# Kernel optimization log

Measured on AMD Instinct MI355X. Metric: run time of the kernel, lower is better.

The kernel has to match this reference:

```python
import jax, jax.numpy as jnp
import numpy as np

C = 192   # channels (class attr)
N = 196   # tokens per stream; 2N = 392, R feat dim = 784
B = 256

def _pw(x, w, b):
    # 1x1 Conv1d == pointwise channel mix: x [B,Ci,L] -> [B,Co,L]
    return jnp.einsum('oi,bil->bol', w, x) + b[None, :, None]

def _bn(x, g, beta, m, v):
    # eval-mode BatchNorm1d
    inv = g / jnp.sqrt(v + 1e-5)
    return (x - m[None, :, None]) * inv[None, :, None] + beta[None, :, None]

def setup_inputs():
    key = jax.random.key(0)
    ks = jax.random.split(key, 24)
    s = 1.0 / np.sqrt(C)
    d = {}
    d['x'] = jax.random.normal(ks[0], (B, N, C), dtype=jnp.float32)
    d['y'] = jax.random.normal(ks[1], (B, N, C), dtype=jnp.float32)
    # linear_conv_1: Conv1d(C,C,1) + BN + ReLU
    d['w1'] = jax.random.normal(ks[2], (C, C), dtype=jnp.float32) * s
    d['b1'] = jax.random.normal(ks[3], (C,), dtype=jnp.float32) * 0.01
    d['g1'] = jnp.ones((C,), jnp.float32)
    d['be1'] = jnp.zeros((C,), jnp.float32)
    d['m1'] = jax.random.normal(ks[4], (C,), dtype=jnp.float32) * 0.1
    d['v1'] = jax.random.uniform(ks[5], (C,), dtype=jnp.float32) + 0.5
    # linear_conv_2
    d['w2'] = jax.random.normal(ks[6], (C, C), dtype=jnp.float32) * s
    d['b2'] = jax.random.normal(ks[7], (C,), dtype=jnp.float32) * 0.01
    d['g2'] = jnp.ones((C,), jnp.float32)
    d['be2'] = jnp.zeros((C,), jnp.float32)
    d['m2'] = jax.random.normal(ks[8], (C,), dtype=jnp.float32) * 0.1
    d['v2'] = jax.random.uniform(ks[9], (C,), dtype=jnp.float32) + 0.5
    # linear_conv_3: Conv1d(C,C,1)
    d['w3'] = jax.random.normal(ks[10], (C, C), dtype=jnp.float32) * s
    d['b3'] = jax.random.normal(ks[11], (C,), dtype=jnp.float32) * 0.01
    # linear_conv_4: Conv1d(784,784,1)
    d['w4'] = jax.random.normal(ks[12], (784, 784), dtype=jnp.float32) / np.sqrt(784)
    d['b4'] = jax.random.normal(ks[13], (784,), dtype=jnp.float32) * 0.01
    # linear_conv_5: Conv1d(C+784,1,1)
    d['w5'] = jax.random.normal(ks[14], (1, C + 784), dtype=jnp.float32) / np.sqrt(C + 784)
    d['b5'] = jax.random.normal(ks[15], (1,), dtype=jnp.float32) * 0.01
    return d

def reference(x, y, w1, b1, g1, be1, m1, v1, w2, b2, g2, be2, m2, v2, w3, b3, w4, b4, w5, b5):
    xp = jnp.swapaxes(x, 1, 2)  # [B,C,N]
    yp = jnp.swapaxes(y, 1, 2)
    phi_x = jax.nn.relu(_bn(_pw(xp, w1, b1), g1, be1, m1, v1))
    phi_y = jax.nn.relu(_bn(_pw(yp, w2, b2), g2, be2, m2, v2))
    cat_phi = jnp.concatenate([phi_x, phi_y], axis=2)            # [B,C,2N]
    A = jnp.einsum('bcn,bcm->bnm', cat_phi, cat_phi)             # [B,2N,2N]
    # R[b,i,:] = cat(A[b,i,:], A[b,:,i]) for i in 0..2N-1, then permute(0,2,1)
    R = jnp.concatenate([A, jnp.swapaxes(A, 1, 2)], axis=2)      # [B,2N,4N]
    R = jnp.swapaxes(R, 1, 2)                                    # [B,4N,2N] = [B,784,392]
    v = _pw(cat_phi, w3, b3)                                     # [B,C,392]
    v_ = _pw(R, w4, b4)                                          # [B,784,392]
    cat_v = jnp.concatenate([v, v_], axis=1)                     # [B,976,392]
    W = _pw(cat_v, w5, b5)                                       # [B,1,392]
    out = xp * W[:, :, :N] + yp * W[:, :, N:]                    # [B,C,N]
    return out
```

## Files before the change

### kernel.cpp

```cpp
#include <hip/hip_runtime.h>
#include <hip/hip_bf16.h>

typedef __attribute__((ext_vector_type(8))) short bf16x8;
typedef __attribute__((ext_vector_type(4))) float f32x4;

#define CDIM 192
#define NTOK 196
#define LTOT 392
#define NBE 64

__device__ __forceinline__ ushort f2bf(float f) {
  uint u = __float_as_uint(f);
  u = (u + 0x7FFFu + ((u >> 16) & 1u)) >> 16;
  return (ushort)u;
}
__device__ __forceinline__ float bf2f(ushort h) {
  return __uint_as_float(((uint)h) << 16);
}
__device__ __forceinline__ uint pk2(float lo, float hi) {
  __hip_bfloat162 t = __float22bfloat162_rn(float2{lo, hi});
  uint r;
  __builtin_memcpy(&r, &t, 4);
  return r;
}
__device__ __forceinline__ float wave_reduce(float a) {
#pragma unroll
  for (int off = 32; off > 0; off >>= 1) a += __shfl_xor(a, off);
  return a;
}
__device__ __forceinline__ void barL() {
  asm volatile("s_waitcnt lgkmcnt(0)" ::: "memory");
  __builtin_amdgcn_s_barrier();
  __builtin_amdgcn_sched_barrier(0);
}

__global__ __launch_bounds__(256) void prep_kernel(
    const float* __restrict__ w1, const float* __restrict__ b1, const float* __restrict__ g1,
    const float* __restrict__ be1, const float* __restrict__ m1, const float* __restrict__ v1,
    const float* __restrict__ w2, const float* __restrict__ b2, const float* __restrict__ g2,
    const float* __restrict__ be2, const float* __restrict__ m2, const float* __restrict__ v2,
    const float* __restrict__ w3, const float* __restrict__ b3,
    const float* __restrict__ w4, const float* __restrict__ b4,
    const float* __restrict__ w5, const float* __restrict__ b5,
    ushort* __restrict__ w1b, ushort* __restrict__ w2b,
    float* __restrict__ u3, float* __restrict__ u4, float* __restrict__ cvecs,
    float* __restrict__ Kc) {
  const int bid = blockIdx.x;
  const int wid = threadIdx.x >> 6, lane = threadIdx.x & 63;
  if (bid < NBE) {
    for (int i = bid * 256 + threadIdx.x; i < 74112; i += NBE * 256) {
      if (i < 36864) {
        int o = i / CDIM;
        float inv = g1[o] * rsqrtf(v1[o] + 1e-5f);
        w1b[i] = f2bf(w1[i] * inv);
      } else if (i < 73728) {
        int j = i - 36864; int o = j / CDIM;
        float inv = g2[o] * rsqrtf(v2[o] + 1e-5f);
        w2b[j] = f2bf(w2[j] * inv);
      } else {
        int k = i - 73728; int h = k / CDIM, o = k % CDIM;
        const float* bb = h ? b2 : b1; const float* gg = h ? g2 : g1;
        const float* bee = h ? be2 : be1;
        const float* mm = h ? m2 : m1; const float* vv = h ? v2 : v1;
        float inv = gg[o] * rsqrtf(vv[o] + 1e-5f);
        cvecs[k] = (bb[o] - mm[o]) * inv + bee[o];
      }
    }
  } else if (bid < NBE + 48) {
    int j = (bid - NBE) * 4 + wid;
    float a = 0.f;
    for (int c = lane; c < CDIM; c += 64) a += w5[c] * w3[c * CDIM + j];
    a = wave_reduce(a);
    if (lane == 0) u3[j] = a;
  } else if (bid < NBE + 48 + 98) {
    int j = (bid - NBE - 48) * 4 + wid;
    float a = 0.f;
    for (int o = lane; o < 784; o += 64)
      a += w5[CDIM + o] * (w4[o * 784 + j] + w4[o * 784 + j + LTOT]);
    a = wave_reduce(a);
    if (lane == 0) u4[j] = a;
  } else {
    if (wid == 0) {
      float a = 0.f;
      for (int i = lane; i < CDIM + 784; i += 64)
        a += (i < CDIM) ? w5[i] * b3[i] : w5[i] * b4[i - CDIM];
      a = wave_reduce(a);
      if (lane == 0) Kc[0] = a + b5[0];
    }
  }
}

#define PHIL_BYTES (404 * 384)
#define OFF_U4S PHIL_BYTES
#define OFF_CSL (OFF_U4S + 1632)
#define OFF_SARR (OFF_CSL + 1536)
#define OFF_WL (OFF_SARR + 768)
#define SMEM_BYTES (OFF_WL + 1568)

extern __shared__ char smem[];

__global__ __launch_bounds__(768, 1) void fused_kernel(
    const float* __restrict__ x, const float* __restrict__ y,
    const ushort* __restrict__ w1b, const ushort* __restrict__ w2b,
    const float* __restrict__ cvecs, const float* __restrict__ u4,
    const float* __restrict__ u3, const float* __restrict__ Kc,
    float* __restrict__ out) {
  const int b = blockIdx.x;
  ushort* phiL = (ushort*)smem;
  float* u4s = (float*)(smem + OFF_U4S);
  float* csL = (float*)(smem + OFF_CSL);
  float* sArr = (float*)(smem + OFF_SARR);
  float* Wl = (float*)(smem + OFF_WL);
  const int tid = threadIdx.x;
  for (int i = tid; i < 408; i += 768) u4s[i] = (i < LTOT) ? u4[i] : 0.f;
  for (int i = tid; i < 384; i += 768) csL[i] = cvecs[i];

  const int w = tid >> 6, lane = tid & 63;
  const int lrow = lane & 15, kgrp = lane >> 4;
  const int c = w * 16 + lrow;

  bf16x8 bfr0[6], bfr1[6];
#pragma unroll
  for (int kk = 0; kk < 6; kk++) {
    bfr0[kk] = *(const bf16x8*)(w1b + (size_t)c * CDIM + kk * 32 + kgrp * 8);
    bfr1[kk] = *(const bf16x8*)(w2b + (size_t)c * CDIM + kk * 32 + kgrp * 8);
  }
  barL();
  const float csr0 = csL[c], csr1 = csL[CDIM + c];

  const float4* xb4 = (const float4*)(x + (size_t)b * NTOK * CDIM);
  const float4* yb4 = (const float4*)(y + (size_t)b * NTOK * CDIM);
  float sp = 0.f;

  auto loadpf = [&](int R, float4* pf) {
    if (R < 8) {
      const float4* s4 = (R < 4) ? xb4 : yb4;
      const int base = (R & 3) * 3072;
#pragma unroll
      for (int p = 0; p < 4; p++) {
        const int fi = base + p * 768 + tid;
        pf[p] = (fi < 9408) ? s4[fi] : float4{0.f, 0.f, 0.f, 0.f};
      }
    }
  };
  float4 pfA[4], pfB[4];
  loadpf(0, pfA);
  loadpf(1, pfB);

  for (int R = 0; R < 8; R++) {
    const int h = R >> 2, r = R & 3;
#pragma unroll
    for (int p = 0; p < 4; p++) {
      const int fi = r * 3072 + p * 768 + tid;
      if (fi < 9408) {
        const int row = fi / 48, c4 = fi - row * 48;
        const int l = h * NTOK + row;
        uint2 wv;
        wv.x = pk2(pfA[p].x, pfA[p].y);
        wv.y = pk2(pfA[p].z, pfA[p].w);
        uint addr = (uint)(l * 384 + c4 * 8) ^ (uint)((l & 7) << 4);
        *(uint2*)((char*)phiL + addr) = wv;
      }
    }
#pragma unroll
    for (int p = 0; p < 4; p++) pfA[p] = pfB[p];
    loadpf(R + 2, pfB);
    barL();

    f32x4 acc[4];
#pragma unroll
    for (int tt = 0; tt < 4; tt++) acc[tt] = f32x4{0.f, 0.f, 0.f, 0.f};
#pragma unroll
    for (int tt = 0; tt < 4; tt++) {
      const int rb = r * 64 + tt * 16;
      if (rb < NTOK) {
        bf16x8 af[6];
        const int l0 = h * NTOK + rb + lrow;
#pragma unroll
        for (int kk = 0; kk < 6; kk++) {
          uint ad = (uint)(l0 * 384 + (kk * 32 + kgrp * 8) * 2) ^ (uint)((l0 & 7) << 4);
          af[kk] = *(const bf16x8*)((const char*)phiL + ad);
        }
        if (h == 0) {
#pragma unroll
          for (int kk = 0; kk < 6; kk++)
            acc[tt] = __builtin_amdgcn_mfma_f32_16x16x32_bf16(af[kk], bfr0[kk], acc[tt], 0, 0, 0);
        } else {
#pragma unroll
          for (int kk = 0; kk < 6; kk++)
            acc[tt] = __builtin_amdgcn_mfma_f32_16x16x32_bf16(af[kk], bfr1[kk], acc[tt], 0, 0, 0);
        }
      }
    }
    barL();

    const float csr = h ? csr1 : csr0;
#pragma unroll
    for (int tt = 0; tt < 4; tt++) {
      const int rb = r * 64 + tt * 16;
      if (rb < NTOK) {
        const float v0 = fmaxf(acc[tt][0] + csr, 0.f);
        const float v1 = fmaxf(acc[tt][1] + csr, 0.f);
        const float v2 = fmaxf(acc[tt][2] + csr, 0.f);
        const float v3 = fmaxf(acc[tt][3] + csr, 0.f);
        const uint p01 = pk2(v0, v1), p23 = pk2(v2, v3);
        const int row0 = rb + 4 * kgrp;
#pragma unroll
        for (int j = 0; j < 4; j++) {
          const int row = row0 + j;
          if (row < NTOK) {
            const int l = h * NTOK + row;
            uint addr = (uint)(l * 384 + c * 2) ^ (uint)((l & 7) << 4);
            const uint piece = (j == 0) ? (p01 & 0xFFFFu) : (j == 1) ? (p01 >> 16)
                             : (j == 2) ? (p23 & 0xFFFFu) : (p23 >> 16);
            *(ushort*)((char*)phiL + addr) = (ushort)piece;
            const float vj = (j == 0) ? v0 : (j == 1) ? v1 : (j == 2) ? v2 : v3;
            sp += u4s[l] * vj;
          }
        }
      }
    }
  }

  sp += __shfl_xor(sp, 16);
  sp += __shfl_xor(sp, 32);
  if (kgrp == 0) sArr[c] = sp;
  barL();
  for (int i = tid; i < CDIM; i += 768) sArr[i] = u3[i] + sArr[i];
  barL();

  const float Kv = Kc[0];
  const int grp = tid >> 2, g4 = tid & 3;
  for (int l = grp; l < LTOT; l += 192) {
    float acc = 0.f;
#pragma unroll
    for (int q = 0; q < 12; q++) {
      const int cc = g4 * 48 + q * 4;
      uint addr = (uint)(l * 384 + cc * 2) ^ (uint)((l & 7) << 4);
      ushort4 v = *(const ushort4*)((const char*)phiL + addr);
      acc += sArr[cc] * bf2f(v.x) + sArr[cc + 1] * bf2f(v.y) +
             sArr[cc + 2] * bf2f(v.z) + sArr[cc + 3] * bf2f(v.w);
    }
    acc += __shfl_xor(acc, 1);
    acc += __shfl_xor(acc, 2);
    if (g4 == 0) Wl[l] = acc + Kv;
  }

  float* tileF = (float*)smem;
  const float* xb = x + (size_t)b * NTOK * CDIM;
  const float* yb = y + (size_t)b * NTOK * CDIM;
  float4 px[2], py[2];
  auto loadT = [&](int nt) {
    if (nt < 7) {
#pragma unroll
      for (int p = 0; p < 2; p++) {
        const int i = p * 768 + tid;
        if (i < 1344) {
          const size_t xi = (size_t)(nt * 28 + i / 48) * CDIM + (i % 48) * 4;
          px[p] = *(const float4*)&xb[xi];
          py[p] = *(const float4*)&yb[xi];
        }
      }
    }
  };
  loadT(0);
  for (int nt = 0; nt < 7; nt++) {
    const int n0 = nt * 28;
    barL();
#pragma unroll
    for (int p = 0; p < 2; p++) {
      const int i = p * 768 + tid;
      if (i < 1344) {
        const int nl = i / 48, c4 = (i % 48) * 4;
        const float wx = Wl[n0 + nl], wy = Wl[NTOK + n0 + nl];
        tileF[nl * 193 + c4 + 0] = px[p].x * wx + py[p].x * wy;
        tileF[nl * 193 + c4 + 1] = px[p].y * wx + py[p].y * wy;
        tileF[nl * 193 + c4 + 2] = px[p].z * wx + py[p].z * wy;
        tileF[nl * 193 + c4 + 3] = px[p].w * wx + py[p].w * wy;
      }
    }
    loadT(nt + 1);
    barL();
#pragma unroll
    for (int p = 0; p < 2; p++) {
      const int i = p * 768 + tid;
      if (i < 1344) {
        const int cc = i / 7, nq = i % 7;
        float4 o;
        o.x = tileF[(nq * 4 + 0) * 193 + cc];
        o.y = tileF[(nq * 4 + 1) * 193 + cc];
        o.z = tileF[(nq * 4 + 2) * 193 + cc];
        o.w = tileF[(nq * 4 + 3) * 193 + cc];
        *(float4*)&out[((size_t)b * CDIM + cc) * NTOK + n0 + nq * 4] = o;
      }
    }
  }
}

extern "C" void kernel_launch(void* const* d_in, const int* in_sizes, int n_in,
                              void* d_out, int out_size, void* d_ws, size_t ws_size,
                              hipStream_t stream) {
  const float* x   = (const float*)d_in[0];
  const float* y   = (const float*)d_in[1];
  const float* w1  = (const float*)d_in[2];
  const float* b1  = (const float*)d_in[3];
  const float* g1  = (const float*)d_in[4];
  const float* be1 = (const float*)d_in[5];
  const float* m1  = (const float*)d_in[6];
  const float* v1  = (const float*)d_in[7];
  const float* w2  = (const float*)d_in[8];
  const float* b2  = (const float*)d_in[9];
  const float* g2  = (const float*)d_in[10];
  const float* be2 = (const float*)d_in[11];
  const float* m2  = (const float*)d_in[12];
  const float* v2  = (const float*)d_in[13];
  const float* w3  = (const float*)d_in[14];
  const float* b3  = (const float*)d_in[15];
  const float* w4  = (const float*)d_in[16];
  const float* b4  = (const float*)d_in[17];
  const float* w5  = (const float*)d_in[18];
  const float* b5  = (const float*)d_in[19];
  float* out = (float*)d_out;

  char* ws = (char*)d_ws;
  ushort* w1b  = (ushort*)ws;
  ushort* w2b  = (ushort*)(ws + 73728);
  float* fbase = (float*)(ws + 147456);
  float* u3    = fbase;
  float* u4    = fbase + 192;
  float* cvecs = fbase + 584;
  float* Kc    = fbase + 968;

  prep_kernel<<<211, 256, 0, stream>>>(w1, b1, g1, be1, m1, v1,
                                       w2, b2, g2, be2, m2, v2,
                                       w3, b3, w4, b4, w5, b5,
                                       w1b, w2b, u3, u4, cvecs, Kc);
  fused_kernel<<<256, 768, SMEM_BYTES, stream>>>(x, y, w1b, w2b, cvecs, u4,
                                                 u3, Kc, out);
}
```

Baseline: 61.37 us.

## Restructure phi stage into four large chunks with deeper prefetch and vectorized W pass

```diff
diff --git a/kernel.cpp b/kernel.cpp
--- a/kernel.cpp
+++ b/kernel.cpp
@@ -119,108 +119,98 @@
   const int lrow = lane & 15, kgrp = lane >> 4;
   const int c = w * 16 + lrow;
 
-  bf16x8 bfr0[6], bfr1[6];
-#pragma unroll
-  for (int kk = 0; kk < 6; kk++) {
-    bfr0[kk] = *(const bf16x8*)(w1b + (size_t)c * CDIM + kk * 32 + kgrp * 8);
-    bfr1[kk] = *(const bf16x8*)(w2b + (size_t)c * CDIM + kk * 32 + kgrp * 8);
-  }
-  barL();
-  const float csr0 = csL[c], csr1 = csL[CDIM + c];
+  bf16x8 bfr[6];
+#pragma unroll
+  for (int kk = 0; kk < 6; kk++)
+    bfr[kk] = *(const bf16x8*)(w1b + (size_t)c * CDIM + kk * 32 + kgrp * 8);
 
   const float4* xb4 = (const float4*)(x + (size_t)b * NTOK * CDIM);
   const float4* yb4 = (const float4*)(y + (size_t)b * NTOK * CDIM);
+  float4 pfA[7], pfB[6];
   float sp = 0.f;
 
-  auto loadpf = [&](int R, float4* pf) {
-    if (R < 8) {
-      const float4* s4 = (R < 4) ? xb4 : yb4;
-      const int base = (R & 3) * 3072;
-#pragma unroll
-      for (int p = 0; p < 4; p++) {
-        const int fi = base + p * 768 + tid;
-        pf[p] = (fi < 9408) ? s4[fi] : float4{0.f, 0.f, 0.f, 0.f};
-      }
-    }
-  };
-  float4 pfA[4], pfB[4];
-  loadpf(0, pfA);
-  loadpf(1, pfB);
-
-  for (int R = 0; R < 8; R++) {
-    const int h = R >> 2, r = R & 3;
-#pragma unroll
-    for (int p = 0; p < 4; p++) {
-      const int fi = r * 3072 + p * 768 + tid;
-      if (fi < 9408) {
-        const int row = fi / 48, c4 = fi - row * 48;
-        const int l = h * NTOK + row;
-        uint2 wv;
-        wv.x = pk2(pfA[p].x, pfA[p].y);
-        wv.y = pk2(pfA[p].z, pfA[p].w);
-        uint addr = (uint)(l * 384 + c4 * 8) ^ (uint)((l & 7) << 4);
-        *(uint2*)((char*)phiL + addr) = wv;
-      }
-    }
-#pragma unroll
-    for (int p = 0; p < 4; p++) pfA[p] = pfB[p];
-    loadpf(R + 2, pfB);
-    barL();
-
-    f32x4 acc[4];
-#pragma unroll
-    for (int tt = 0; tt < 4; tt++) acc[tt] = f32x4{0.f, 0.f, 0.f, 0.f};
-#pragma unroll
-    for (int tt = 0; tt < 4; tt++) {
-      const int rb = r * 64 + tt * 16;
-      if (rb < NTOK) {
-        bf16x8 af[6];
-        const int l0 = h * NTOK + rb + lrow;
-#pragma unroll
-        for (int kk = 0; kk < 6; kk++) {
-          uint ad = (uint)(l0 * 384 + (kk * 32 + kgrp * 8) * 2) ^ (uint)((l0 & 7) << 4);
-          af[kk] = *(const bf16x8*)((const char*)phiL + ad);
-        }
-        if (h == 0) {
-#pragma unroll
-          for (int kk = 0; kk < 6; kk++)
-            acc[tt] = __builtin_amdgcn_mfma_f32_16x16x32_bf16(af[kk], bfr0[kk], acc[tt], 0, 0, 0);
-        } else {
-#pragma unroll
-          for (int kk = 0; kk < 6; kk++)
-            acc[tt] = __builtin_amdgcn_mfma_f32_16x16x32_bf16(af[kk], bfr1[kk], acc[tt], 0, 0, 0);
-        }
-      }
-    }
-    barL();
-
-    const float csr = h ? csr1 : csr0;
-#pragma unroll
-    for (int tt = 0; tt < 4; tt++) {
-      const int rb = r * 64 + tt * 16;
-      if (rb < NTOK) {
-        const float v0 = fmaxf(acc[tt][0] + csr, 0.f);
-        const float v1 = fmaxf(acc[tt][1] + csr, 0.f);
-        const float v2 = fmaxf(acc[tt][2] + csr, 0.f);
-        const float v3 = fmaxf(acc[tt][3] + csr, 0.f);
-        const uint p01 = pk2(v0, v1), p23 = pk2(v2, v3);
-        const int row0 = rb + 4 * kgrp;
-#pragma unroll
-        for (int j = 0; j < 4; j++) {
-          const int row = row0 + j;
-          if (row < NTOK) {
-            const int l = h * NTOK + row;
-            uint addr = (uint)(l * 384 + c * 2) ^ (uint)((l & 7) << 4);
-            const uint piece = (j == 0) ? (p01 & 0xFFFFu) : (j == 1) ? (p01 >> 16)
-                             : (j == 2) ? (p23 & 0xFFFFu) : (p23 >> 16);
-            *(ushort*)((char*)phiL + addr) = (ushort)piece;
-            const float vj = (j == 0) ? v0 : (j == 1) ? v1 : (j == 2) ? v2 : v3;
-            sp += u4s[l] * vj;
-          }
-        }
-      }
-    }
-  }
+#define LOADC(PF, CNT, NF4, SRC4, ROW0) do {                                   \
+  _Pragma("unroll")                                                            \
+  for (int p = 0; p < (CNT); p++) {                                            \
+    const int fi = p * 768 + tid;                                              \
+    (PF)[p] = (fi < (NF4)) ? (SRC4)[(ROW0) * 48 + fi]                          \
+                           : float4{0.f, 0.f, 0.f, 0.f};                       \
+  } } while (0)
+
+#define STAGE(PF, CNT, NF4, H, ROW0) do {                                      \
+  _Pragma("unroll")                                                            \
+  for (int p = 0; p < (CNT); p++) {                                            \
+    const int fi = p * 768 + tid;                                              \
+    if (fi < (NF4)) {                                                          \
+      const int l = (H) * NTOK + (ROW0) + fi / 48;                             \
+      const int c4 = fi % 48;                                                  \
+      uint2 wv;                                                                \
+      wv.x = pk2((PF)[p].x, (PF)[p].y);                                        \
+      wv.y = pk2((PF)[p].z, (PF)[p].w);                                        \
+      uint addr = (uint)(l * 384 + c4 * 8) ^ (uint)((l & 7) << 4);             \
+      *(uint2*)((char*)phiL + addr) = wv;                                      \
+    } } } while (0)
+
+#define MFMA_EPI(H, ROW0, NT, CSR) do {                                        \
+  f32x4 acc[7];                                                                \
+  _Pragma("unroll")                                                            \
+  for (int tt = 0; tt < 7; tt++) acc[tt] = f32x4{0.f, 0.f, 0.f, 0.f};          \
+  _Pragma("unroll")                                                            \
+  for (int tt = 0; tt < 7; tt++) if (tt < (NT)) {                              \
+    const int l0 = (H) * NTOK + (ROW0) + tt * 16 + lrow;                       \
+    bf16x8 af[6];                                                              \
+    _Pragma("unroll")                                                          \
+    for (int kk = 0; kk < 6; kk++) {                                           \
+      uint ad = (uint)(l0 * 384 + kk * 64 + kgrp * 16) ^ (uint)((l0 & 7) << 4);\
+      af[kk] = *(const bf16x8*)((const char*)phiL + ad);                       \
+    }                                                                          \
+    _Pragma("unroll")                                                          \
+    for (int kk = 0; kk < 6; kk++)                                             \
+      acc[tt] = __builtin_amdgcn_mfma_f32_16x16x32_bf16(af[kk], bfr[kk],       \
+                                                        acc[tt], 0, 0, 0);    \
+  }                                                                            \
+  barL();                \
+  _Pragma("unroll")                                                            \
+  for (int tt = 0; tt < 7; tt++) if (tt < (NT)) {                              \
+    const float v0 = fmaxf(acc[tt][0] + (CSR), 0.f);                           \
+    const float v1 = fmaxf(acc[tt][1] + (CSR), 0.f);                           \
+    const float v2 = fmaxf(acc[tt][2] + (CSR), 0.f);                           \
+    const float v3 = fmaxf(acc[tt][3] + (CSR), 0.f);                           \
+    const uint p01 = pk2(v0, v1), p23 = pk2(v2, v3);                           \
+    const int rw0 = (ROW0) + tt * 16 + 4 * kgrp;                               \
+    _Pragma("unroll")                                                          \
+    for (int j = 0; j < 4; j++) {                                              \
+      const int row = rw0 + j;                                                 \
+      if (row < NTOK) {                                                        \
+        const int l = (H) * NTOK + row;                                        \
+        uint addr = (uint)(l * 384 + c * 2) ^ (uint)((l & 7) << 4);            \
+        const uint piece = (j == 0) ? (p01 & 0xFFFFu) : (j == 1) ? (p01 >> 16) \
+                         : (j == 2) ? (p23 & 0xFFFFu) : (p23 >> 16);           \
+        *(ushort*)((char*)phiL + addr) = (ushort)piece;                        \
+        const float vj = (j == 0) ? v0 : (j == 1) ? v1 : (j == 2) ? v2 : v3;   \
+        sp += u4s[l] * vj;                                                     \
+      } } } } while (0)
+
+  LOADC(pfA, 7, 5376, xb4, 0);
+  LOADC(pfB, 6, 4032, xb4, 112);
+  STAGE(pfA, 7, 5376, 0, 0);
+  LOADC(pfA, 7, 5376, yb4, 0);
+  barL();
+  const float csr0 = csL[c], csr1 = csL[CDIM + c];
+  MFMA_EPI(0, 0, 7, csr0);
+  STAGE(pfB, 6, 4032, 0, 112);
+  LOADC(pfB, 6, 4032, yb4, 112);
+  barL();
+  MFMA_EPI(0, 112, 6, csr0);
+#pragma unroll
+  for (int kk = 0; kk < 6; kk++)
+    bfr[kk] = *(const bf16x8*)(w2b + (size_t)c * CDIM + kk * 32 + kgrp * 8);
+  STAGE(pfA, 7, 5376, 1, 0);
+  barL();
+  MFMA_EPI(1, 0, 7, csr1);
+  STAGE(pfB, 6, 4032, 1, 112);
+  barL();
+  MFMA_EPI(1, 112, 6, csr1);
 
   sp += __shfl_xor(sp, 16);
   sp += __shfl_xor(sp, 32);
@@ -230,56 +220,67 @@
   barL();
 
   const float Kv = Kc[0];
-  const int grp = tid >> 2, g4 = tid & 3;
-  for (int l = grp; l < LTOT; l += 192) {
+#pragma unroll
+  for (int p = 0; p < 3; p++) {
+    const int row = p * 192 + w * 16 + lrow;
     float acc = 0.f;
-#pragma unroll
-    for (int q = 0; q < 12; q++) {
-      const int cc = g4 * 48 + q * 4;
-      uint addr = (uint)(l * 384 + cc * 2) ^ (uint)((l & 7) << 4);
-      ushort4 v = *(const ushort4*)((const char*)phiL + addr);
-      acc += sArr[cc] * bf2f(v.x) + sArr[cc + 1] * bf2f(v.y) +
-             sArr[cc + 2] * bf2f(v.z) + sArr[cc + 3] * bf2f(v.w);
+    if (row < LTOT) {
+#pragma unroll
+      for (int kk = 0; kk < 6; kk++) {
+        const int c0 = kk * 32 + kgrp * 8;
+        uint addr = (uint)(row * 384 + c0 * 2) ^ (uint)((row & 7) << 4);
+        const uint4 pv = *(const uint4*)((const char*)phiL + addr);
+        const float4 cfa = *(const float4*)&sArr[c0];
+        const float4 cfb = *(const float4*)&sArr[c0 + 4];
+        acc += cfa.x * bf2f((ushort)pv.x) + cfa.y * bf2f((ushort)(pv.x >> 16))
+             + cfa.z * bf2f((ushort)pv.y) + cfa.w * bf2f((ushort)(pv.y >> 16))
+             + cfb.x * bf2f((ushort)pv.z) + cfb.y * bf2f((ushort)(pv.z >> 16))
+             + cfb.z * bf2f((ushort)pv.w) + cfb.w * bf2f((ushort)(pv.w >> 16));
+      }
     }
-    acc += __shfl_xor(acc, 1);
-    acc += __shfl_xor(acc, 2);
-    if (g4 == 0) Wl[l] = acc + Kv;
+    acc += __shfl_xor(acc, 16);
+    acc += __shfl_xor(acc, 32);
+    if (kgrp == 0 && row < LTOT) Wl[row] = acc + Kv;
   }
 
   float* tileF = (float*)smem;
   const float* xb = x + (size_t)b * NTOK * CDIM;
   const float* yb = y + (size_t)b * NTOK * CDIM;
-  float4 px[2], py[2];
-  auto loadT = [&](int nt) {
-    if (nt < 7) {
-#pragma unroll
-      for (int p = 0; p < 2; p++) {
-        const int i = p * 768 + tid;
-        if (i < 1344) {
-          const size_t xi = (size_t)(nt * 28 + i / 48) * CDIM + (i % 48) * 4;
-          px[p] = *(const float4*)&xb[xi];
-          py[p] = *(const float4*)&yb[xi];
-        }
-      }
-    }
-  };
-  loadT(0);
+  float4 pxA[2], pyA[2], pxB[2], pyB[2];
+
+#define LOADT(NT, PX, PY) do {                                                 \
+  if ((NT) < 7) {                                                              \
+    _Pragma("unroll")                                                          \
+    for (int p = 0; p < 2; p++) {                                              \
+      const int i = p * 768 + tid;                                             \
+      if (i < 1344) {                                                          \
+        const size_t xi = (size_t)((NT) * 28 + i / 48) * CDIM + (i % 48) * 4;  \
+        (PX)[p] = *(const float4*)&xb[xi];                                     \
+        (PY)[p] = *(const float4*)&yb[xi];                                     \
+      } } } } while (0)
+
+#define COMBINE(N0, PX, PY) do {                                               \
+  _Pragma("unroll")                                                            \
+  for (int p = 0; p < 2; p++) {                                                \
+    const int i = p * 768 + tid;                                               \
+    if (i < 1344) {                                                            \
+      const int nl = i / 48, c4 = (i % 48) * 4;                                \
+      const float wx = Wl[(N0) + nl], wy = Wl[NTOK + (N0) + nl];               \
+      float4 o;                                                                \
+      o.x = (PX)[p].x * wx + (PY)[p].x * wy;                                   \
+      o.y = (PX)[p].y * wx + (PY)[p].y * wy;                                   \
+      o.z = (PX)[p].z * wx + (PY)[p].z * wy;                                   \
+      o.w = (PX)[p].w * wx + (PY)[p].w * wy;                                   \
+      *(float4*)&tileF[nl * 196 + c4] = o;                                     \
+    } } } while (0)
+
+  LOADT(0, pxA, pyA);
+  LOADT(1, pxB, pyB);
   for (int nt = 0; nt < 7; nt++) {
     const int n0 = nt * 28;
     barL();
-#pragma unroll
-    for (int p = 0; p < 2; p++) {
-      const int i = p * 768 + tid;
-      if (i < 1344) {
-        const int nl = i / 48, c4 = (i % 48) * 4;
-        const float wx = Wl[n0 + nl], wy = Wl[NTOK + n0 + nl];
-        tileF[nl * 193 + c4 + 0] = px[p].x * wx + py[p].x * wy;
-        tileF[nl * 193 + c4 + 1] = px[p].y * wx + py[p].y * wy;
-        tileF[nl * 193 + c4 + 2] = px[p].z * wx + py[p].z * wy;
-        tileF[nl * 193 + c4 + 3] = px[p].w * wx + py[p].w * wy;
-      }
-    }
-    loadT(nt + 1);
+    if (nt & 1) { COMBINE(n0, pxB, pyB); LOADT(nt + 2, pxB, pyB); }
+    else        { COMBINE(n0, pxA, pyA); LOADT(nt + 2, pxA, pyA); }
     barL();
 #pragma unroll
     for (int p = 0; p < 2; p++) {
@@ -287,10 +288,10 @@
       if (i < 1344) {
         const int cc = i / 7, nq = i % 7;
         float4 o;
-        o.x = tileF[(nq * 4 + 0) * 193 + cc];
-        o.y = tileF[(nq * 4 + 1) * 193 + cc];
-        o.z = tileF[(nq * 4 + 2) * 193 + cc];
-        o.w = tileF[(nq * 4 + 3) * 193 + cc];
+        o.x = tileF[(nq * 4 + 0) * 196 + cc];
+        o.y = tileF[(nq * 4 + 1) * 196 + cc];
+        o.z = tileF[(nq * 4 + 2) * 196 + cc];
+        o.w = tileF[(nq * 4 + 3) * 196 + cc];
         *(float4*)&out[((size_t)b * CDIM + cc) * NTOK + n0 + nq * 4] = o;
       }
     }
```

Result: no change. 61.11 us, median of 2 (-0.4%).

## Restructure fused kernel with 32x32 MFMA tiles, half-stream chunks, per-wave output transpose

Applied to the files above, without the earlier changes.

```diff
diff --git a/kernel.cpp b/kernel.cpp
--- a/kernel.cpp
+++ b/kernel.cpp
@@ -2,7 +2,7 @@
 #include <hip/hip_bf16.h>
 
 typedef __attribute__((ext_vector_type(8))) short bf16x8;
-typedef __attribute__((ext_vector_type(4))) float f32x4;
+typedef __attribute__((ext_vector_type(16))) float f32x16;
 
 #define CDIM 192
 #define NTOK 196
@@ -90,12 +90,12 @@
   }
 }
 
-#define PHIL_BYTES (404 * 384)
-#define OFF_U4S PHIL_BYTES
+#define OFF_WL 0
+#define OFF_PHIL 1568
+#define OFF_U4S (OFF_PHIL + 150528)
 #define OFF_CSL (OFF_U4S + 1632)
-#define OFF_SARR (OFF_CSL + 1536)
-#define OFF_WL (OFF_SARR + 768)
-#define SMEM_BYTES (OFF_WL + 1568)
+#define OFF_SA (OFF_CSL + 1536)
+#define SMEM_BYTES (OFF_SA + 1536)
 
 extern __shared__ char smem[];
 
@@ -106,192 +106,196 @@
     const float* __restrict__ u3, const float* __restrict__ Kc,
     float* __restrict__ out) {
   const int b = blockIdx.x;
-  ushort* phiL = (ushort*)smem;
+  float* Wl = (float*)(smem + OFF_WL);
+  char* phiB = smem + OFF_PHIL;
   float* u4s = (float*)(smem + OFF_U4S);
   float* csL = (float*)(smem + OFF_CSL);
-  float* sArr = (float*)(smem + OFF_SARR);
-  float* Wl = (float*)(smem + OFF_WL);
+  float* sA = (float*)(smem + OFF_SA);
   const int tid = threadIdx.x;
   for (int i = tid; i < 408; i += 768) u4s[i] = (i < LTOT) ? u4[i] : 0.f;
   for (int i = tid; i < 384; i += 768) csL[i] = cvecs[i];
 
   const int w = tid >> 6, lane = tid & 63;
-  const int lrow = lane & 15, kgrp = lane >> 4;
-  const int c = w * 16 + lrow;
-
-  bf16x8 bfr0[6], bfr1[6];
-#pragma unroll
-  for (int kk = 0; kk < 6; kk++) {
-    bfr0[kk] = *(const bf16x8*)(w1b + (size_t)c * CDIM + kk * 32 + kgrp * 8);
-    bfr1[kk] = *(const bf16x8*)(w2b + (size_t)c * CDIM + kk * 32 + kgrp * 8);
-  }
-  barL();
-  const float csr0 = csL[c], csr1 = csL[CDIM + c];
+  const int cw = w % 6, lg = w / 6;
+  const int cbase = cw * 32;
+  const int cl32 = lane & 31, hi = lane >> 5;
+  const int c = cbase + cl32;
+
+  bf16x8 bfr[12];
+#pragma unroll
+  for (int kk = 0; kk < 12; kk++)
+    bfr[kk] = *(const bf16x8*)(w1b + (size_t)c * CDIM + kk * 16 + hi * 8);
 
   const float4* xb4 = (const float4*)(x + (size_t)b * NTOK * CDIM);
   const float4* yb4 = (const float4*)(y + (size_t)b * NTOK * CDIM);
+  float4 pfA[6], pfB[7];
   float sp = 0.f;
 
-  auto loadpf = [&](int R, float4* pf) {
-    if (R < 8) {
-      const float4* s4 = (R < 4) ? xb4 : yb4;
-      const int base = (R & 3) * 3072;
-#pragma unroll
-      for (int p = 0; p < 4; p++) {
-        const int fi = base + p * 768 + tid;
-        pf[p] = (fi < 9408) ? s4[fi] : float4{0.f, 0.f, 0.f, 0.f};
-      }
-    }
-  };
-  float4 pfA[4], pfB[4];
-  loadpf(0, pfA);
-  loadpf(1, pfB);
-
-  for (int R = 0; R < 8; R++) {
-    const int h = R >> 2, r = R & 3;
-#pragma unroll
-    for (int p = 0; p < 4; p++) {
-      const int fi = r * 3072 + p * 768 + tid;
-      if (fi < 9408) {
-        const int row = fi / 48, c4 = fi - row * 48;
+  auto loadA = [&](const float4* s4) {
+#pragma unroll
+    for (int p = 0; p < 6; p++) pfA[p] = s4[p * 768 + tid];
+  };
+  auto loadB = [&](const float4* s4) {
+#pragma unroll
+    for (int p = 0; p < 7; p++) {
+      const int fi = p * 768 + tid;
+      pfB[p] = (fi < 4800) ? s4[4608 + fi] : float4{0.f, 0.f, 0.f, 0.f};
+    }
+  };
+  auto stageA = [&](int h) {
+#pragma unroll
+    for (int p = 0; p < 6; p++) {
+      const int fi = p * 768 + tid;
+      const int l = h * NTOK + fi / 48, c4 = fi % 48;
+      uint2 wv;
+      wv.x = pk2(pfA[p].x, pfA[p].y);
+      wv.y = pk2(pfA[p].z, pfA[p].w);
+      uint addr = (uint)(l * 384 + c4 * 8) ^ (uint)((l & 7) << 4);
+      *(uint2*)(phiB + addr) = wv;
+    }
+  };
+  auto stageB = [&](int h) {
+#pragma unroll
+    for (int p = 0; p < 7; p++) {
+      const int fi = p * 768 + tid;
+      if (fi < 4800) {
+        const int l = h * NTOK + 96 + fi / 48, c4 = fi % 48;
+        uint2 wv;
+        wv.x = pk2(pfB[p].x, pfB[p].y);
+        wv.y = pk2(pfB[p].z, pfB[p].w);
+        uint addr = (uint)(l * 384 + c4 * 8) ^ (uint)((l & 7) << 4);
+        *(uint2*)(phiB + addr) = wv;
+      }
+    }
+  };
+
+  auto tileMFMA = [&](int h, int l0) -> f32x16 {
+    f32x16 acc;
+#pragma unroll
+    for (int e = 0; e < 16; e++) acc[e] = 0.f;
+    const int l = h * NTOK + l0 + cl32;
+    const uint swz = (uint)((l & 7) << 4);
+#pragma unroll
+    for (int kk = 0; kk < 12; kk++) {
+      uint ad = (uint)(l * 384 + kk * 32 + hi * 16) ^ swz;
+      bf16x8 af = *(const bf16x8*)(phiB + ad);
+      acc = __builtin_amdgcn_mfma_f32_32x32x16_bf16(af, bfr[kk], acc, 0, 0, 0);
+    }
+    return acc;
+  };
+  auto tileEPI = [&](int h, int l0, const f32x16& acc, float csr, bool ovl) {
+#pragma unroll
+    for (int e = 0; e < 16; e++) {
+      const int rl = (e & 3) + 8 * (e >> 2) + 4 * hi;
+      const int row = l0 + rl;
+      if (!ovl || row >= 192) {
+        const float v = fmaxf(acc[e] + csr, 0.f);
         const int l = h * NTOK + row;
-        uint2 wv;
-        wv.x = pk2(pfA[p].x, pfA[p].y);
-        wv.y = pk2(pfA[p].z, pfA[p].w);
-        uint addr = (uint)(l * 384 + c4 * 8) ^ (uint)((l & 7) << 4);
-        *(uint2*)((char*)phiL + addr) = wv;
-      }
-    }
-#pragma unroll
-    for (int p = 0; p < 4; p++) pfA[p] = pfB[p];
-    loadpf(R + 2, pfB);
+        uint addr = (uint)(l * 384 + c * 2) ^ (uint)((l & 7) << 4);
+        *(ushort*)(phiB + addr) = f2bf(v);
+        sp += u4s[l] * v;
+      }
+    }
+  };
+  auto chunkCompute = [&](int h, int cb, float csr) {
+    const int l0s[2][4] = {{0, 32, 64, -1}, {96, 128, 160, 164}};
+    const int nt = cb ? 4 : 3;
+    f32x16 a0, a1;
+    const int t0 = lg, t1 = lg + 2;
+    if (t0 < nt) a0 = tileMFMA(h, l0s[cb][t0]);
+    if (t1 < nt) a1 = tileMFMA(h, l0s[cb][t1]);
     barL();
-
-    f32x4 acc[4];
-#pragma unroll
-    for (int tt = 0; tt < 4; tt++) acc[tt] = f32x4{0.f, 0.f, 0.f, 0.f};
-#pragma unroll
-    for (int tt = 0; tt < 4; tt++) {
-      const int rb = r * 64 + tt * 16;
-      if (rb < NTOK) {
-        bf16x8 af[6];
-        const int l0 = h * NTOK + rb + lrow;
+    if (t0 < nt) tileEPI(h, l0s[cb][t0], a0, csr, cb && l0s[cb][t0] == 164);
+    if (t1 < nt) tileEPI(h, l0s[cb][t1], a1, csr, cb && l0s[cb][t1] == 164);
+  };
+
+  loadA(xb4);
+  loadB(xb4);
+  stageA(0);
+  loadA(yb4);
+  barL();
+  const float csr0 = csL[c], csr1 = csL[CDIM + c];
+  chunkCompute(0, 0, csr0);
+  stageB(0);
+  loadB(yb4);
+  barL();
+  chunkCompute(0, 1, csr0);
+#pragma unroll
+  for (int kk = 0; kk < 12; kk++)
+    bfr[kk] = *(const bf16x8*)(w2b + (size_t)c * CDIM + kk * 16 + hi * 8);
+  stageA(1);
+  barL();
+  chunkCompute(1, 0, csr1);
+  stageB(1);
+  barL();
+  chunkCompute(1, 1, csr1);
+
+  sp += __shfl_xor(sp, 32);
+  if (hi == 0) sA[lg * CDIM + c] = sp;
+  barL();
+  for (int i = tid; i < CDIM; i += 768) sA[i] = u3[i] + sA[i] + sA[CDIM + i];
+  barL();
+
+  {
+    const float Kv = Kc[0];
+    const int lrow = lane & 15, kgrp = lane >> 4;
+#pragma unroll
+    for (int p = 0; p < 3; p++) {
+      const int row = p * 192 + w * 16 + lrow;
+      float acc = 0.f;
+      if (row < LTOT) {
 #pragma unroll
         for (int kk = 0; kk < 6; kk++) {
-          uint ad = (uint)(l0 * 384 + (kk * 32 + kgrp * 8) * 2) ^ (uint)((l0 & 7) << 4);
-          af[kk] = *(const bf16x8*)((const char*)phiL + ad);
+          const int c0 = kk * 32 + kgrp * 8;
+          uint addr = (uint)(row * 384 + c0 * 2) ^ (uint)((row & 7) << 4);
+          const uint4 pv = *(const uint4*)(phiB + addr);
+          const float4 cfa = *(const float4*)&sA[c0];
+          const float4 cfb = *(const float4*)&sA[c0 + 4];
+          acc += cfa.x * bf2f((ushort)pv.x) + cfa.y * bf2f((ushort)(pv.x >> 16))
+               + cfa.z * bf2f((ushort)pv.y) + cfa.w * bf2f((ushort)(pv.y >> 16))
+               + cfb.x * bf2f((ushort)pv.z) + cfb.y * bf2f((ushort)(pv.z >> 16))
+               + cfb.z * bf2f((ushort)pv.w) + cfb.w * bf2f((ushort)(pv.w >> 16));
         }
-        if (h == 0) {
-#pragma unroll
-          for (int kk = 0; kk < 6; kk++)
-            acc[tt] = __builtin_amdgcn_mfma_f32_16x16x32_bf16(af[kk], bfr0[kk], acc[tt], 0, 0, 0);
-        } else {
-#pragma unroll
-          for (int kk = 0; kk < 6; kk++)
-            acc[tt] = __builtin_amdgcn_mfma_f32_16x16x32_bf16(af[kk], bfr1[kk], acc[tt], 0, 0, 0);
+      }
+      acc += __shfl_xor(acc, 16);
+      acc += __shfl_xor(acc, 32);
+      if (kgrp == 0 && row < LTOT) Wl[row] = acc + Kv;
+    }
+  }
+  barL();
+
+  {
+    float* tf = (float*)(phiB + w * 4352);
+    const int cb16 = w * 16;
+    const float* xb = x + (size_t)b * NTOK * CDIM;
+    const float* yb = y + (size_t)b * NTOK * CDIM;
+    const int nrow = lane >> 2, cq = lane & 3;
+    const int scl = lane >> 2, sq = lane & 3;
+    for (int s0 = 0; s0 < 4; s0++) {
+      const int n0 = s0 * 64;
+#pragma unroll
+      for (int i2 = 0; i2 < 4; i2++) {
+        const int n = n0 + i2 * 16 + nrow;
+        if (n < NTOK) {
+          const size_t xi = (size_t)n * CDIM + cb16 + cq * 4;
+          const float4 xv = *(const float4*)&xb[xi];
+          const float4 yv = *(const float4*)&yb[xi];
+          const float wx = Wl[n], wy = Wl[NTOK + n];
+          const int dn = n - n0;
+          tf[(cq * 4 + 0) * 68 + dn] = xv.x * wx + yv.x * wy;
+          tf[(cq * 4 + 1) * 68 + dn] = xv.y * wx + yv.y * wy;
+          tf[(cq * 4 + 2) * 68 + dn] = xv.z * wx + yv.z * wy;
+          tf[(cq * 4 + 3) * 68 + dn] = xv.w * wx + yv.w * wy;
         }
       }
-    }
-    barL();
-
-    const float csr = h ? csr1 : csr0;
-#pragma unroll
-    for (int tt = 0; tt < 4; tt++) {
-      const int rb = r * 64 + tt * 16;
-      if (rb < NTOK) {
-        const float v0 = fmaxf(acc[tt][0] + csr, 0.f);
-        const float v1 = fmaxf(acc[tt][1] + csr, 0.f);
-        const float v2 = fmaxf(acc[tt][2] + csr, 0.f);
-        const float v3 = fmaxf(acc[tt][3] + csr, 0.f);
-        const uint p01 = pk2(v0, v1), p23 = pk2(v2, v3);
-        const int row0 = rb + 4 * kgrp;
-#pragma unroll
-        for (int j = 0; j < 4; j++) {
-          const int row = row0 + j;
-          if (row < NTOK) {
-            const int l = h * NTOK + row;
-            uint addr = (uint)(l * 384 + c * 2) ^ (uint)((l & 7) << 4);
-            const uint piece = (j == 0) ? (p01 & 0xFFFFu) : (j == 1) ? (p01 >> 16)
-                             : (j == 2) ? (p23 & 0xFFFFu) : (p23 >> 16);
-            *(ushort*)((char*)phiL + addr) = (ushort)piece;
-            const float vj = (j == 0) ? v0 : (j == 1) ? v1 : (j == 2) ? v2 : v3;
-            sp += u4s[l] * vj;
-          }
+      asm volatile("s_waitcnt lgkmcnt(0)" ::: "memory");
+#pragma unroll
+      for (int i2 = 0; i2 < 4; i2++) {
+        const int n = n0 + i2 * 16 + sq * 4;
+        if (n < NTOK) {
+          const float4 o = *(const float4*)&tf[scl * 68 + (n - n0)];
+          *(float4*)&out[((size_t)b * CDIM + cb16 + scl) * NTOK + n] = o;
         }
-      }
-    }
-  }
-
-  sp += __shfl_xor(sp, 16);
-  sp += __shfl_xor(sp, 32);
-  if (kgrp == 0) sArr[c] = sp;
-  barL();
-  for (int i = tid; i < CDIM; i += 768) sArr[i] = u3[i] + sArr[i];
-  barL();
-
-  const float Kv = Kc[0];
-  const int grp = tid >> 2, g4 = tid & 3;
-  for (int l = grp; l < LTOT; l += 192) {
-    float acc = 0.f;
-#pragma unroll
-    for (int q = 0; q < 12; q++) {
-      const int cc = g4 * 48 + q * 4;
-      uint addr = (uint)(l * 384 + cc * 2) ^ (uint)((l & 7) << 4);
-      ushort4 v = *(const ushort4*)((const char*)phiL + addr);
-      acc += sArr[cc] * bf2f(v.x) + sArr[cc + 1] * bf2f(v.y) +
-             sArr[cc + 2] * bf2f(v.z) + sArr[cc + 3] * bf2f(v.w);
-    }
-    acc += __shfl_xor(acc, 1);
-    acc += __shfl_xor(acc, 2);
-    if (g4 == 0) Wl[l] = acc + Kv;
-  }
-
-  float* tileF = (float*)smem;
-  const float* xb = x + (size_t)b * NTOK * CDIM;
-  const float* yb = y + (size_t)b * NTOK * CDIM;
-  float4 px[2], py[2];
-  auto loadT = [&](int nt) {
-    if (nt < 7) {
-#pragma unroll
-      for (int p = 0; p < 2; p++) {
-        const int i = p * 768 + tid;
-        if (i < 1344) {
-          const size_t xi = (size_t)(nt * 28 + i / 48) * CDIM + (i % 48) * 4;
-          px[p] = *(const float4*)&xb[xi];
-          py[p] = *(const float4*)&yb[xi];
-        }
-      }
-    }
-  };
-  loadT(0);
-  for (int nt = 0; nt < 7; nt++) {
-    const int n0 = nt * 28;
-    barL();
-#pragma unroll
-    for (int p = 0; p < 2; p++) {
-      const int i = p * 768 + tid;
-      if (i < 1344) {
-        const int nl = i / 48, c4 = (i % 48) * 4;
-        const float wx = Wl[n0 + nl], wy = Wl[NTOK + n0 + nl];
-        tileF[nl * 193 + c4 + 0] = px[p].x * wx + py[p].x * wy;
-        tileF[nl * 193 + c4 + 1] = px[p].y * wx + py[p].y * wy;
-        tileF[nl * 193 + c4 + 2] = px[p].z * wx + py[p].z * wy;
-        tileF[nl * 193 + c4 + 3] = px[p].w * wx + py[p].w * wy;
-      }
-    }
-    loadT(nt + 1);
-    barL();
-#pragma unroll
-    for (int p = 0; p < 2; p++) {
-      const int i = p * 768 + tid;
-      if (i < 1344) {
-        const int cc = i / 7, nq = i % 7;
-        float4 o;
-        o.x = tileF[(nq * 4 + 0) * 193 + cc];
-        o.y = tileF[(nq * 4 + 1) * 193 + cc];
-        o.z = tileF[(nq * 4 + 2) * 193 + cc];
-        o.w = tileF[(nq * 4 + 3) * 193 + cc];
-        *(float4*)&out[((size_t)b * CDIM + cc) * NTOK + n0 + nq * 4] = o;
       }
     }
   }
```

Measured after the change: 61.80 us. No clear change (+0.7%).
